# Performance work log

Measured on AMD Instinct MI355X. Metric: run time of the kernel, lower is better.

The kernel has to match this reference:

```python
import jax, jax.numpy as jnp
import numpy as np

B = 2_000_000
L = 64
STEPS = 10
LAT_CONST = 5 * 0.03 / 200 + 0.06  # queue*lat/bw + 0.06
GRAD_CONST = 1.0 / 0.06
SEND_CONST = 2.0 / 3.0


def setup_inputs() -> dict:
    key = jax.random.key(0)
    ks = jax.random.split(key, 5)
    x = jax.random.normal(ks[0], (B, 7), dtype=jnp.float32)
    # column 0 is the loop counter i; program assumes it starts at 0 -> 10 iterations
    x = x.at[:, 0].set(0.0)
    W1 = jax.random.normal(ks[1], (3, L), dtype=jnp.float32) * 0.1
    b1 = jnp.zeros((L,), dtype=jnp.float32)
    W2 = jax.random.normal(ks[2], (L, L), dtype=jnp.float32) * 0.1
    b2 = jnp.zeros((L,), dtype=jnp.float32)
    W3 = jax.random.normal(ks[3], (L, 1), dtype=jnp.float32) * 0.1
    b3 = jnp.zeros((1,), dtype=jnp.float32)
    return {"x": x, "W1": W1, "b1": b1, "W2": W2, "b2": b2, "W3": W3, "b3": b3}


def _mlp(feat, W1, b1, W2, b2, W3, b3):
    h = jax.nn.relu(feat @ W1 + b1)
    h = jax.nn.relu(h @ W2 + b2)
    return jax.nn.sigmoid(h @ W3 + b3)[:, 0]


def reference(x, W1, b1, W2, b2, W3, b3):
    def step(state, _):
        x2 = state[:, 2]
        x6 = state[:, 6]
        # IfElse on column 6 vs comparison_bar=0.0:
        #   body  (x6 <= 0): x2 * (x6 + 1)          (assign_upper_sender_ratio)
        #   else  (x6 >  0): x2 * ((1 - x6) / 1)    (assign_down_sender_ratio, sub_l = left-sub)
        x2 = jnp.where(x6 <= 0.0, x2 * (x6 + 1.0), x2 * (1.0 - x6))
        x4 = x2 + LAT_CONST            # latency_ratio
        x5 = x2 * SEND_CONST           # sending_ratio
        x3 = x4 * GRAD_CONST           # latency_gradient
        feat = jnp.stack([x3, x4, x5], axis=1)  # [B,3]
        a = _mlp(feat, W1, b1, W2, b2, W3, b3)  # new action -> column 2
        new_state = state.at[:, 0].add(1.0)
        new_state = new_state.at[:, 2].set(a)
        new_state = new_state.at[:, 3].set(x3)
        new_state = new_state.at[:, 4].set(x4)
        new_state = new_state.at[:, 5].set(x5)
        return new_state, None

    final, _ = jax.lax.scan(step, x, None, length=STEPS)
    return final
```

## Files before the change

kernel.cpp:

```cpp
#include <hip/hip_runtime.h>
#include <math.h>

#define LAT_CONST  ((float)(5.0 * 0.03 / 200.0 + 0.06))
#define GRAD_CONST ((float)(1.0 / 0.06))
#define SEND_CONST ((float)(2.0 / 3.0))

#define NW   2048
#define LOW_ (-24.f)
#define HIW_ (24.f)
#define HW_  ((HIW_ - LOW_) / (float)NW)
#define IHW_ ((float)NW / (HIW_ - LOW_))
#define CW_  (-LOW_ * IHW_)
#define N2   2048
#define LO2  (-6.25f)
#define HI2  (1.25f)
#define H2   ((HI2 - LO2) / (float)N2)
#define IH2  ((float)N2 / (HI2 - LO2))
#define C2   (-LO2 * IH2)

#define GSZ   2080
#define GPCK  2064

__global__ __launch_bounds__(256)
void build_table_kernel(const float* __restrict__ W1, const float* __restrict__ b1,
                        const float* __restrict__ W2, const float* __restrict__ b2,
                        const float* __restrict__ W3, const float* __restrict__ b3,
                        float* __restrict__ g1, float* __restrict__ g2)
{
    __shared__ float pl[4][64];

    const int lane = threadIdx.x & 63;
    const int w    = threadIdx.x >> 6;
    const int i    = blockIdx.x * 64 + lane;

    float t;
    if (i < GSZ) t = LOW_ + (float)i * HW_;
    else         t = LO2 + (float)(i - GSZ) * H2;

    float x4 = t + LAT_CONST;
    float x5 = t * SEND_CONST;
    float x3 = x4 * GRAD_CONST;

    float h1v[64];
#pragma unroll
    for (int j = 0; j < 64; ++j) {
        float acc = b1[j];
        acc = fmaf(x3, W1[j],       acc);
        acc = fmaf(x4, W1[64 + j],  acc);
        acc = fmaf(x5, W1[128 + j], acc);
        h1v[j] = fmaxf(acc, 0.f);
    }

    const int j0 = w * 16;
    float acc[16];
#pragma unroll
    for (int u = 0; u < 16; ++u) acc[u] = b2[j0 + u];
#pragma unroll
    for (int k = 0; k < 64; ++k) {
        const float* __restrict__ w2r = W2 + k * 64 + j0;
#pragma unroll
        for (int u = 0; u < 16; ++u)
            acc[u] = fmaf(h1v[k], w2r[u], acc[u]);
    }
    float partial = 0.f;
#pragma unroll
    for (int u = 0; u < 16; ++u)
        partial = fmaf(fmaxf(acc[u], 0.f), W3[j0 + u], partial);

    pl[w][lane] = partial;
    __syncthreads();

    if (w == 0) {
        float logit = b3[0] + ((pl[0][lane] + pl[1][lane]) + (pl[2][lane] + pl[3][lane]));
        float g = 1.f / (1.f + expf(-logit));
        if (i < GSZ) g1[i] = g;
        else         g2[i - GSZ] = g;
    }
}

#define CHUNK 256
#define BLOCK 256
#define MAXBLK 1792

typedef unsigned int u32;
typedef __attribute__((address_space(3))) u32 lds_u32_t;
typedef __attribute__((address_space(1))) const u32 glb_u32_t;

__device__ __forceinline__ void gload16(const void* g, void* l) {
    __builtin_amdgcn_global_load_lds((glb_u32_t*)g, (lds_u32_t*)l, 16, 0, 0);
}
__device__ __forceinline__ void gload4(const void* g, void* l) {
    __builtin_amdgcn_global_load_lds((glb_u32_t*)g, (lds_u32_t*)l, 4, 0, 0);
}

__device__ __forceinline__ u32 bfpack(float a, float b) {
    u32 ua = __float_as_uint(a), ub = __float_as_uint(b);
    ua = (ua + 0x7fffu + ((ua >> 16) & 1u)) >> 16;
    ub = (ub + 0x7fffu + ((ub >> 16) & 1u)) & 0xffff0000u;
    return (ua & 0xffffu) | ub;
}

__device__ __forceinline__ float lerp_pk(u32 u, float fr) {
    float e0 = __uint_as_float(u << 16);
    float e1 = __uint_as_float(u & 0xffff0000u);
    return fmaf(e1 - e0, fr, e0);
}

__global__ __launch_bounds__(BLOCK)
void rows_kernel(const float* __restrict__ x, const float* __restrict__ g1,
                 const float* __restrict__ g2, float* __restrict__ out,
                 int B, int nChunks, int grid)
{
    __shared__ u32 tn[GPCK];
    __shared__ __align__(16) float buf[2][CHUNK * 7];

    const int tid = threadIdx.x;
    const long long b = blockIdx.x;
    const int cb = (int)(b * (long long)nChunks / grid);
    const int ce = (int)((b + 1) * (long long)nChunks / grid);

    {
        int rows0 = min(CHUNK, B - cb * CHUNK);
        int nfl0  = rows0 * 7;
        int nf40  = nfl0 >> 2;
        const float* src = x + (size_t)cb * CHUNK * 7;
        for (int i = tid; i < nf40; i += BLOCK)
            gload16((const float4*)src + i, &buf[0][i * 4]);
        for (int i = (nf40 << 2) + tid; i < nfl0; i += BLOCK)
            gload4(src + i, &buf[0][i]);
    }
    for (int i = tid; i < GPCK / 4; i += BLOCK) {
        float4 q = ((const float4*)g2)[i];
        float ny = g2[i * 4 + 4];
        tn[i*4+0] = bfpack(q.x, q.y); tn[i*4+1] = bfpack(q.y, q.z);
        tn[i*4+2] = bfpack(q.z, q.w); tn[i*4+3] = bfpack(q.w, ny);
    }
    __syncthreads();

    int cur = 0;
    for (int c = cb; c < ce; ++c) {
        if (c + 1 < ce) {
            int rowsN = min(CHUNK, B - (c + 1) * CHUNK);
            int nflN  = rowsN * 7;
            int nf4N  = nflN >> 2;
            const float* src = x + (size_t)(c + 1) * CHUNK * 7;
            for (int i = tid; i < nf4N; i += BLOCK)
                gload16((const float4*)src + i, &buf[cur ^ 1][i * 4]);
            for (int i = (nf4N << 2) + tid; i < nflN; i += BLOCK)
                gload4(src + i, &buf[cur ^ 1][i]);
        }

        int rows = min(CHUNK, B - c * CHUNK);
        float* bfr = buf[cur];
        for (int r = tid; r < rows; r += BLOCK) {
            float* row = bfr + r * 7;
            float x0 = row[0], x2 = row[2], x6 = row[6];
            float f = (x6 <= 0.f) ? (x6 + 1.f) : (1.f - x6);
            {
                float p = fmaf(x2, f * IHW_, CW_);
                p = fminf(fmaxf(p, 0.f), (float)NW);
                int idx = (int)p; float fr = p - (float)idx;
                float e0 = g1[idx], e1 = g1[idx + 1];
                x2 = fmaf(e1 - e0, fr, e0);
            }
            float af2 = f * IH2;
#pragma unroll
            for (int s = 0; s < 8; ++s) {
                float p = fmaf(x2, af2, C2);
                p = fminf(fmaxf(p, 0.f), (float)N2);
                int idx = (int)p; float fr = p - (float)idx;
                x2 = lerp_pk(tn[idx], fr);
            }
            float t = x2 * f;
            float p = fmaf(t, IH2, C2);
            p = fminf(fmaxf(p, 0.f), (float)N2);
            int idx = (int)p; float fr = p - (float)idx;
            float x2f = lerp_pk(tn[idx], fr);
            float x4 = t + LAT_CONST;
            row[0] = x0 + 10.f;
            row[2] = x2f;
            row[3] = x4 * GRAD_CONST;
            row[4] = x4;
            row[5] = t * SEND_CONST;
        }
        __syncthreads();

        {
            int nfl = rows * 7;
            int nf4 = nfl >> 2;
            float* dst = out + (size_t)c * CHUNK * 7;
            const float4* s4 = (const float4*)bfr;
            for (int i = tid; i < nf4; i += BLOCK) ((float4*)dst)[i] = s4[i];
            for (int i = (nf4 << 2) + tid; i < nfl; i += BLOCK) dst[i] = bfr[i];
        }
        __syncthreads();
        cur ^= 1;
    }
}

static inline size_t align16h(size_t v) { return (v + 15) & ~(size_t)15; }

extern "C" void kernel_launch(void* const* d_in, const int* in_sizes, int n_in,
                              void* d_out, int out_size, void* d_ws, size_t ws_size,
                              hipStream_t stream)
{
    const float* x  = (const float*)d_in[0];
    const float* W1 = (const float*)d_in[1];
    const float* b1 = (const float*)d_in[2];
    const float* W2 = (const float*)d_in[3];
    const float* b2 = (const float*)d_in[4];
    const float* W3 = (const float*)d_in[5];
    const float* b3 = (const float*)d_in[6];
    float* out = (float*)d_out;

    int B = in_sizes[0] / 7;

    char* ws = (char*)d_ws;
    float* g1 = (float*)ws;
    float* g2 = (float*)(ws + align16h((size_t)GSZ * 4));

    int nChunks = (B + CHUNK - 1) / CHUNK;
    int grid    = (nChunks < MAXBLK) ? nChunks : MAXBLK;

    hipLaunchKernelGGL(build_table_kernel, dim3((2 * GSZ) / 64), dim3(256), 0, stream,
                       W1, b1, W2, b2, W3, b3, g1, g2);
    hipLaunchKernelGGL(rows_kernel, dim3(grid), dim3(BLOCK), 0, stream,
                       x, g1, g2, out, B, nChunks, grid);
}
```

Baseline: 39.65 us.

## Prepack bf16 tables in a separate kernel and split lookups between LDS and global

Adds a pack kernel that converts both sigmoid tables into packed bf16 pairs once, so each rows block copies the LDS table with plain uint4 loads instead of repacking it. The first g1 lookup now uses a single packed global load rather than two float loads. Odd iterations of the 8-step loop read from the global packed table instead of LDS, which spreads lookups across the cache and LDS paths. The table build kernel goes to 512 threads with 8 outputs per wave. In exchange it adds a third kernel launch, and g1 is now interpolated from bf16, which lowers its precision.

```diff
diff --git a/kernel.cpp b/kernel.cpp
--- a/kernel.cpp
+++ b/kernel.cpp
@@ -21,13 +21,28 @@
 #define GSZ   2080
 #define GPCK  2064
 
-__global__ __launch_bounds__(256)
+typedef unsigned int u32;
+
+__device__ __forceinline__ u32 bfpack(float a, float b) {
+    u32 ua = __float_as_uint(a), ub = __float_as_uint(b);
+    ua = (ua + 0x7fffu + ((ua >> 16) & 1u)) >> 16;
+    ub = (ub + 0x7fffu + ((ub >> 16) & 1u)) & 0xffff0000u;
+    return (ua & 0xffffu) | ub;
+}
+
+__device__ __forceinline__ float lerp_pk(u32 u, float fr) {
+    float e0 = __uint_as_float(u << 16);
+    float e1 = __uint_as_float(u & 0xffff0000u);
+    return fmaf(e1 - e0, fr, e0);
+}
+
+__global__ __launch_bounds__(512)
 void build_table_kernel(const float* __restrict__ W1, const float* __restrict__ b1,
                         const float* __restrict__ W2, const float* __restrict__ b2,
                         const float* __restrict__ W3, const float* __restrict__ b3,
                         float* __restrict__ g1, float* __restrict__ g2)
 {
-    __shared__ float pl[4][64];
+    __shared__ float pl[8][64];
 
     const int lane = threadIdx.x & 63;
     const int w    = threadIdx.x >> 6;
@@ -51,38 +66,49 @@
         h1v[j] = fmaxf(acc, 0.f);
     }
 
-    const int j0 = w * 16;
-    float acc[16];
-#pragma unroll
-    for (int u = 0; u < 16; ++u) acc[u] = b2[j0 + u];
+    const int j0 = w * 8;
+    float acc[8];
+#pragma unroll
+    for (int u = 0; u < 8; ++u) acc[u] = b2[j0 + u];
 #pragma unroll
     for (int k = 0; k < 64; ++k) {
         const float* __restrict__ w2r = W2 + k * 64 + j0;
 #pragma unroll
-        for (int u = 0; u < 16; ++u)
+        for (int u = 0; u < 8; ++u)
             acc[u] = fmaf(h1v[k], w2r[u], acc[u]);
     }
     float partial = 0.f;
 #pragma unroll
-    for (int u = 0; u < 16; ++u)
+    for (int u = 0; u < 8; ++u)
         partial = fmaf(fmaxf(acc[u], 0.f), W3[j0 + u], partial);
 
     pl[w][lane] = partial;
     __syncthreads();
 
     if (w == 0) {
-        float logit = b3[0] + ((pl[0][lane] + pl[1][lane]) + (pl[2][lane] + pl[3][lane]));
+        float logit = b3[0] + (((pl[0][lane] + pl[1][lane]) + (pl[2][lane] + pl[3][lane]))
+                             + ((pl[4][lane] + pl[5][lane]) + (pl[6][lane] + pl[7][lane])));
         float g = 1.f / (1.f + expf(-logit));
         if (i < GSZ) g1[i] = g;
         else         g2[i - GSZ] = g;
     }
 }
 
+__global__ __launch_bounds__(256)
+void pack_table_kernel(const float* __restrict__ g1, const float* __restrict__ g2,
+                       u32* __restrict__ g1p, u32* __restrict__ g2p)
+{
+    int i = blockIdx.x * blockDim.x + threadIdx.x;
+    if (i < GPCK) {
+        g1p[i] = bfpack(g1[i], g1[i + 1]);
+        g2p[i] = bfpack(g2[i], g2[i + 1]);
+    }
+}
+
 #define CHUNK 256
 #define BLOCK 256
 #define MAXBLK 1792
 
-typedef unsigned int u32;
 typedef __attribute__((address_space(3))) u32 lds_u32_t;
 typedef __attribute__((address_space(1))) const u32 glb_u32_t;
 
@@ -93,22 +119,9 @@
     __builtin_amdgcn_global_load_lds((glb_u32_t*)g, (lds_u32_t*)l, 4, 0, 0);
 }
 
-__device__ __forceinline__ u32 bfpack(float a, float b) {
-    u32 ua = __float_as_uint(a), ub = __float_as_uint(b);
-    ua = (ua + 0x7fffu + ((ua >> 16) & 1u)) >> 16;
-    ub = (ub + 0x7fffu + ((ub >> 16) & 1u)) & 0xffff0000u;
-    return (ua & 0xffffu) | ub;
-}
-
-__device__ __forceinline__ float lerp_pk(u32 u, float fr) {
-    float e0 = __uint_as_float(u << 16);
-    float e1 = __uint_as_float(u & 0xffff0000u);
-    return fmaf(e1 - e0, fr, e0);
-}
-
 __global__ __launch_bounds__(BLOCK)
-void rows_kernel(const float* __restrict__ x, const float* __restrict__ g1,
-                 const float* __restrict__ g2, float* __restrict__ out,
+void rows_kernel(const float* __restrict__ x, const u32* __restrict__ g1p,
+                 const u32* __restrict__ g2p, float* __restrict__ out,
                  int B, int nChunks, int grid)
 {
     __shared__ u32 tn[GPCK];
@@ -129,12 +142,8 @@
         for (int i = (nf40 << 2) + tid; i < nfl0; i += BLOCK)
             gload4(src + i, &buf[0][i]);
     }
-    for (int i = tid; i < GPCK / 4; i += BLOCK) {
-        float4 q = ((const float4*)g2)[i];
-        float ny = g2[i * 4 + 4];
-        tn[i*4+0] = bfpack(q.x, q.y); tn[i*4+1] = bfpack(q.y, q.z);
-        tn[i*4+2] = bfpack(q.z, q.w); tn[i*4+3] = bfpack(q.w, ny);
-    }
+    for (int i = tid; i < GPCK / 4; i += BLOCK)
+        ((uint4*)tn)[i] = ((const uint4*)g2p)[i];
     __syncthreads();
 
     int cur = 0;
@@ -160,8 +169,7 @@
                 float p = fmaf(x2, f * IHW_, CW_);
                 p = fminf(fmaxf(p, 0.f), (float)NW);
                 int idx = (int)p; float fr = p - (float)idx;
-                float e0 = g1[idx], e1 = g1[idx + 1];
-                x2 = fmaf(e1 - e0, fr, e0);
+                x2 = lerp_pk(g1p[idx], fr);
             }
             float af2 = f * IH2;
 #pragma unroll
@@ -169,7 +177,8 @@
                 float p = fmaf(x2, af2, C2);
                 p = fminf(fmaxf(p, 0.f), (float)N2);
                 int idx = (int)p; float fr = p - (float)idx;
-                x2 = lerp_pk(tn[idx], fr);
+                u32 u = (s & 1) ? g2p[idx] : tn[idx];
+                x2 = lerp_pk(u, fr);
             }
             float t = x2 * f;
             float p = fmaf(t, IH2, C2);
@@ -216,14 +225,18 @@
     int B = in_sizes[0] / 7;
 
     char* ws = (char*)d_ws;
-    float* g1 = (float*)ws;
-    float* g2 = (float*)(ws + align16h((size_t)GSZ * 4));
+    float* g1  = (float*)ws;
+    float* g2  = (float*)(ws + align16h((size_t)GSZ * 4));
+    u32*   g1p = (u32*)  (ws + 2 * align16h((size_t)GSZ * 4));
+    u32*   g2p = (u32*)  (ws + 3 * align16h((size_t)GSZ * 4));
 
     int nChunks = (B + CHUNK - 1) / CHUNK;
     int grid    = (nChunks < MAXBLK) ? nChunks : MAXBLK;
 
-    hipLaunchKernelGGL(build_table_kernel, dim3((2 * GSZ) / 64), dim3(256), 0, stream,
+    hipLaunchKernelGGL(build_table_kernel, dim3((2 * GSZ) / 64), dim3(512), 0, stream,
                        W1, b1, W2, b2, W3, b3, g1, g2);
+    hipLaunchKernelGGL(pack_table_kernel, dim3((GPCK + 255) / 256), dim3(256), 0, stream,
+                       g1, g2, g1p, g2p);
     hipLaunchKernelGGL(rows_kernel, dim3(grid), dim3(BLOCK), 0, stream,
-                       x, g1, g2, out, B, nChunks, grid);
-}
+                       x, g1p, g2p, out, B, nChunks, grid);
+}
```

Measured after the change: 39.11 us. About the same (-1.4%).
